# Optimization experiments

Measured on AMD Instinct MI355X. Metric: run time of the kernel, lower is better.

The kernel has to match this reference:

```python
import jax, jax.numpy as jnp
import numpy as np

NUM_CAPSULE = 32
DIM_CAPSULE = 16
ROUTINGS = 3
EPS = 1e-7        # K.epsilon()
L2_EPS = 1e-12    # tf.nn.l2_normalize epsilon


def squash(x, axis=-1):
    s = jnp.sum(jnp.square(x), axis=axis, keepdims=True) + EPS
    scale = jnp.sqrt(s) / (0.5 + s)
    return scale * x


def setup_inputs() -> dict:
    key = jax.random.key(0)
    k1, k2 = jax.random.split(key)
    B, N_in, D_in = 64, 2048, 64
    u_vecs = jax.random.normal(k1, (B, N_in, D_in), dtype=jnp.float32)
    # glorot-ish scale for the 1x1 conv kernel (1, D_in, num_capsule*dim_capsule)
    kernel = jax.random.normal(k2, (1, D_in, NUM_CAPSULE * DIM_CAPSULE), dtype=jnp.float32)
    kernel = kernel * np.sqrt(2.0 / (D_in + NUM_CAPSULE * DIM_CAPSULE)).astype(np.float32)
    return {"u_vecs": u_vecs, "kernel": kernel}


def reference(u_vecs, kernel):
    B, N_in, D_in = u_vecs.shape
    # K.conv1d with kernel_size=1 == matmul along the feature dim
    u_hat = jnp.einsum('bnd,dm->bnm', u_vecs, kernel[0])
    # (B, N_in, num_cap, dim_cap) -> (B, num_cap, N_in, dim_cap)
    u_hat = u_hat.reshape(B, N_in, NUM_CAPSULE, DIM_CAPSULE).transpose(0, 2, 1, 3)

    b = jnp.zeros((B, NUM_CAPSULE, N_in), dtype=u_hat.dtype)
    o = None
    for i in range(ROUTINGS):
        c = jax.nn.softmax(b, axis=1)                 # softmax over output capsules
        o = jnp.einsum('bin,binj->bij', c, u_hat)     # (B, num_cap, dim_cap)
        if i < ROUTINGS - 1:
            norm = jnp.sqrt(jnp.maximum(jnp.sum(jnp.square(o), axis=-1, keepdims=True), L2_EPS))
            o = o / norm                              # K.l2_normalize(o, -1)
            b = jnp.einsum('bij,binj->bin', o, u_hat)  # b = <v, u_hat> (non-accumulating)
    return squash(o)
```

## Files before the change

kernel.cpp:

```cpp
#include <hip/hip_runtime.h>
#include <hip/hip_bf16.h>


#define BB 64
#define NN 2048
#define DD 64
#define II 32

typedef __attribute__((ext_vector_type(8)))  short bf16x8;
typedef __attribute__((ext_vector_type(16))) float f32x16;

__device__ __forceinline__ short f2bf(float f) {
    __hip_bfloat16 h = __float2bfloat16(f);
    return *reinterpret_cast<short*>(&h);
}
__device__ __forceinline__ float bf2f(short s) {
    __hip_bfloat16 h = *reinterpret_cast<__hip_bfloat16*>(&s);
    return __bfloat162float(h);
}

__global__ __launch_bounds__(512) void kall(const float* __restrict__ u,
                                            const float* __restrict__ W,
                                            float* __restrict__ out) {
    int b = blockIdx.x;
    int tid = threadIdx.x;
    int wv = tid >> 6;
    int l = tid & 63, h = l >> 5, ln = l & 31;
    int ii = tid >> 4, jj0 = tid & 15;

    __shared__ unsigned short ush[8][2048];
    __shared__ unsigned short usl[8][2048];
    __shared__ float cslab[8][II * 33];
    __shared__ float tlds[II][65];
    __shared__ float wlds[II][68];
    __shared__ float slds[8][DD];
    __shared__ float ssum[DD];
    __shared__ float osh[II][16];

    const float* ubase = u + (size_t)b * NN * DD;

    {
        const float4* up = reinterpret_cast<const float4*>(ubase + (size_t)wv * 256 * DD);
        int r0 = l >> 4, c4 = l & 15;
        float4 a0 = {0.f, 0.f, 0.f, 0.f};
        #pragma unroll 8
        for (int s = 0; s < 64; ++s) {
            float4 v = up[(s * 4 + r0) * 16 + c4];
            a0.x += v.x; a0.y += v.y; a0.z += v.z; a0.w += v.w;
        }
        #pragma unroll
        for (int off = 16; off <= 32; off <<= 1) {
            a0.x += __shfl_xor(a0.x, off);
            a0.y += __shfl_xor(a0.y, off);
            a0.z += __shfl_xor(a0.z, off);
            a0.w += __shfl_xor(a0.w, off);
        }
        if (l < 16) *reinterpret_cast<float4*>(&slds[wv][l * 4]) = a0;
    }
    for (int k = tid; k < II * 65; k += 512) (&tlds[0][0])[k] = 0.f;
    __syncthreads();

    if (tid < DD) {
        float a = 0.f;
        #pragma unroll
        for (int wq = 0; wq < 8; ++wq) a += slds[wq][tid];
        ssum[tid] = a;
    }
    __syncthreads();
    {
        float o = 0.f;
        #pragma unroll 8
        for (int d = 0; d < DD; ++d) o += ssum[d] * W[d * 512 + ii * 16 + jj0];
        o *= (1.0f / 32.0f);
        float ss = o * o;
        #pragma unroll
        for (int off = 8; off >= 1; off >>= 1) ss += __shfl_xor(ss, off, 16);
        osh[ii][jj0] = o / sqrtf(fmaxf(ss, 1e-12f));
    }
    __syncthreads();
    #pragma unroll
    for (int k = 0; k < 4; ++k) {
        int d = jj0 + 16 * k;
        float acc = 0.f;
        #pragma unroll
        for (int j2 = 0; j2 < 16; ++j2)
            acc += W[d * 512 + ii * 16 + j2] * osh[ii][j2];
        wlds[ii][d] = acc;
    }
    __syncthreads();

    for (int it = 0; it < 2; ++it) {
        bf16x8 Aw[4];
        #pragma unroll
        for (int kt = 0; kt < 4; ++kt) {
            const float* p = &wlds[ln][kt * 16 + h * 8];
            #pragma unroll
            for (int e2 = 0; e2 < 8; ++e2) Aw[kt][e2] = f2bf(p[e2]);
        }
        f32x16 G0, G1;
        #pragma unroll
        for (int r = 0; r < 16; ++r) { G0[r] = 0.f; G1[r] = 0.f; }

        for (int tt = 0; tt < 8; ++tt) {
            int n0 = wv * 256 + tt * 32;
            bf16x8 Bh[4], Bl[4];
            #pragma unroll
            for (int kt = 0; kt < 4; ++kt) {
                const float4* p = reinterpret_cast<const float4*>(
                    ubase + (size_t)(n0 + ln) * DD + kt * 16 + h * 8);
                float4 v0 = p[0], v1 = p[1];
                float vf[8] = {v0.x, v0.y, v0.z, v0.w, v1.x, v1.y, v1.z, v1.w};
                #pragma unroll
                for (int e2 = 0; e2 < 8; ++e2) {
                    short hi = f2bf(vf[e2]);
                    Bh[kt][e2] = hi;
                    Bl[kt][e2] = f2bf(vf[e2] - bf2f(hi));
                }
                int d0 = kt * 16 + h * 8;
                int idx = ln * 64 + (d0 ^ ((ln & 7) << 3));
                *reinterpret_cast<bf16x8*>(&ush[wv][idx]) = Bh[kt];
                *reinterpret_cast<bf16x8*>(&usl[wv][idx]) = Bl[kt];
            }
            f32x16 S;
            #pragma unroll
            for (int r = 0; r < 16; ++r) S[r] = 0.f;
            #pragma unroll
            for (int kt = 0; kt < 4; ++kt)
                S = __builtin_amdgcn_mfma_f32_32x32x16_bf16(Aw[kt], Bh[kt], S, 0, 0, 0);
            float m = S[0];
            #pragma unroll
            for (int r = 1; r < 16; ++r) m = fmaxf(m, S[r]);
            m = fmaxf(m, __shfl_xor(m, 32));
            float sum = 0.f, e[16];
            #pragma unroll
            for (int r = 0; r < 16; ++r) { e[r] = __expf(S[r] - m); sum += e[r]; }
            sum += __shfl_xor(sum, 32);
            float inv = 1.f / sum;
            #pragma unroll
            for (int r = 0; r < 16; ++r) {
                int irow = (r & 3) + 8 * (r >> 2) + 4 * h;
                cslab[wv][ln * 33 + irow] = e[r] * inv;
            }
            #pragma unroll
            for (int t2 = 0; t2 < 2; ++t2) {
                bf16x8 Ah, Al;
                #pragma unroll
                for (int q = 0; q < 8; ++q) {
                    float cv = cslab[wv][(t2 * 16 + h * 8 + q) * 33 + ln];
                    short hi = f2bf(cv);
                    Ah[q] = hi;
                    Al[q] = f2bf(cv - bf2f(hi));
                }
                #pragma unroll
                for (int Nt = 0; Nt < 2; ++Nt) {
                    bf16x8 B2h, B2l;
                    #pragma unroll
                    for (int q = 0; q < 8; ++q) {
                        int row = t2 * 16 + h * 8 + q;
                        int idx = row * 64 + ((Nt * 32 + ln) ^ ((row & 7) << 3));
                        B2h[q] = (short)ush[wv][idx];
                        B2l[q] = (short)usl[wv][idx];
                    }
                    if (Nt == 0) {
                        G0 = __builtin_amdgcn_mfma_f32_32x32x16_bf16(Ah, B2h, G0, 0, 0, 0);
                        G0 = __builtin_amdgcn_mfma_f32_32x32x16_bf16(Al, B2h, G0, 0, 0, 0);
                        G0 = __builtin_amdgcn_mfma_f32_32x32x16_bf16(Ah, B2l, G0, 0, 0, 0);
                    } else {
                        G1 = __builtin_amdgcn_mfma_f32_32x32x16_bf16(Ah, B2h, G1, 0, 0, 0);
                        G1 = __builtin_amdgcn_mfma_f32_32x32x16_bf16(Al, B2h, G1, 0, 0, 0);
                        G1 = __builtin_amdgcn_mfma_f32_32x32x16_bf16(Ah, B2l, G1, 0, 0, 0);
                    }
                }
            }
        }
        #pragma unroll
        for (int r = 0; r < 16; ++r) {
            int irow = (r & 3) + 8 * (r >> 2) + 4 * h;
            atomicAdd(&tlds[irow][ln],      G0[r]);
            atomicAdd(&tlds[irow][32 + ln], G1[r]);
        }
        __syncthreads();

        float o = 0.f;
        #pragma unroll 8
        for (int d = 0; d < DD; ++d) o += tlds[ii][d] * W[d * 512 + ii * 16 + jj0];
        float ss = o * o;
        #pragma unroll
        for (int off = 8; off >= 1; off >>= 1) ss += __shfl_xor(ss, off, 16);

        if (it == 0) {
            float ov = o / sqrtf(fmaxf(ss, 1e-12f));
            __syncthreads();
            osh[ii][jj0] = ov;
            __syncthreads();
            #pragma unroll
            for (int k = 0; k < 4; ++k) {
                int d = jj0 + 16 * k;
                float acc = 0.f;
                #pragma unroll
                for (int j2 = 0; j2 < 16; ++j2)
                    acc += W[d * 512 + ii * 16 + j2] * osh[ii][j2];
                wlds[ii][d] = acc;
            }
            for (int k = tid; k < II * 65; k += 512) (&tlds[0][0])[k] = 0.f;
            __syncthreads();
        } else {
            float s2 = ss + 1e-7f;
            float scale = sqrtf(s2) / (0.5f + s2);
            out[(size_t)b * 512 + tid] = scale * o;
        }
    }
}

extern "C" void kernel_launch(void* const* d_in, const int* in_sizes, int n_in,
                              void* d_out, int out_size, void* d_ws, size_t ws_size,
                              hipStream_t stream) {
    const float* u = (const float*)d_in[0];
    const float* W = (const float*)d_in[1];
    float* out = (float*)d_out;
    (void)d_ws; (void)ws_size;

    kall<<<BB, 512, 0, stream>>>(u, W, out);
}
```

Baseline: 100.8 us.

## Split each batch across four cooperative blocks with grid sync reductions

Launches a cooperative kernel with 256 blocks (four per batch element), each handling 512 of the 2048 input rows. Partial column sums and per-iteration routing accumulators go through global workspace and are combined after grid.sync. This targets the low occupancy of the original 64-block launch on a GPU with many more CUs. The cost is three grid-wide barriers plus extra global traffic, and the old kernel is kept as a fallback if the cooperative launch fails. Global loads in the main loop are also batched before conversion.

```diff
diff --git a/kernel.cpp b/kernel.cpp
--- a/kernel.cpp
+++ b/kernel.cpp
@@ -1,5 +1,8 @@
 #include <hip/hip_runtime.h>
 #include <hip/hip_bf16.h>
+#include <hip/hip_cooperative_groups.h>
+
+namespace cg = cooperative_groups;
 
 
 #define BB 64
@@ -19,10 +22,15 @@
     return __bfloat162float(h);
 }
 
-__global__ __launch_bounds__(512) void kall(const float* __restrict__ u,
-                                            const float* __restrict__ W,
-                                            float* __restrict__ out) {
-    int b = blockIdx.x;
+__global__ __launch_bounds__(512) void kco(const float* __restrict__ u,
+                                           const float* __restrict__ W,
+                                           float* __restrict__ out,
+                                           float* __restrict__ sglob,
+                                           float* __restrict__ tglob) {
+    cg::grid_group grid = cg::this_grid();
+
+    int blk = blockIdx.x;
+    int b = blk >> 2, q = blk & 3;
     int tid = threadIdx.x;
     int wv = tid >> 6;
     int l = tid & 63, h = l >> 5, ln = l & 31;
@@ -38,13 +46,14 @@
     __shared__ float osh[II][16];
 
     const float* ubase = u + (size_t)b * NN * DD;
+    int rbase = q * 512 + wv * 64;
 
     {
-        const float4* up = reinterpret_cast<const float4*>(ubase + (size_t)wv * 256 * DD);
+        const float4* up = reinterpret_cast<const float4*>(ubase + (size_t)rbase * DD);
         int r0 = l >> 4, c4 = l & 15;
         float4 a0 = {0.f, 0.f, 0.f, 0.f};
-        #pragma unroll 8
-        for (int s = 0; s < 64; ++s) {
+        #pragma unroll
+        for (int s = 0; s < 16; ++s) {
             float4 v = up[(s * 4 + r0) * 16 + c4];
             a0.x += v.x; a0.y += v.y; a0.z += v.z; a0.w += v.w;
         }
@@ -57,13 +66,20 @@
         }
         if (l < 16) *reinterpret_cast<float4*>(&slds[wv][l * 4]) = a0;
     }
-    for (int k = tid; k < II * 65; k += 512) (&tlds[0][0])[k] = 0.f;
-    __syncthreads();
-
+    __syncthreads();
     if (tid < DD) {
         float a = 0.f;
         #pragma unroll
         for (int wq = 0; wq < 8; ++wq) a += slds[wq][tid];
+        sglob[(size_t)blk * DD + tid] = a;
+    }
+    __threadfence();
+    grid.sync();
+
+    if (tid < DD) {
+        float a = 0.f;
+        #pragma unroll
+        for (int q2 = 0; q2 < 4; ++q2) a += sglob[(size_t)(b * 4 + q2) * DD + tid];
         ssum[tid] = a;
     }
     __syncthreads();
@@ -101,15 +117,21 @@
         #pragma unroll
         for (int r = 0; r < 16; ++r) { G0[r] = 0.f; G1[r] = 0.f; }
 
-        for (int tt = 0; tt < 8; ++tt) {
-            int n0 = wv * 256 + tt * 32;
+        #pragma unroll
+        for (int tt = 0; tt < 2; ++tt) {
+            int n0 = rbase + tt * 32;
             bf16x8 Bh[4], Bl[4];
+            float4 v0[4], v1[4];
             #pragma unroll
             for (int kt = 0; kt < 4; ++kt) {
                 const float4* p = reinterpret_cast<const float4*>(
                     ubase + (size_t)(n0 + ln) * DD + kt * 16 + h * 8);
-                float4 v0 = p[0], v1 = p[1];
-                float vf[8] = {v0.x, v0.y, v0.z, v0.w, v1.x, v1.y, v1.z, v1.w};
+                v0[kt] = p[0]; v1[kt] = p[1];
+            }
+            #pragma unroll
+            for (int kt = 0; kt < 4; ++kt) {
+                float vf[8] = {v0[kt].x, v0[kt].y, v0[kt].z, v0[kt].w,
+                               v1[kt].x, v1[kt].y, v1[kt].z, v1[kt].w};
                 #pragma unroll
                 for (int e2 = 0; e2 < 8; ++e2) {
                     short hi = f2bf(vf[e2]);
@@ -145,21 +167,21 @@
             for (int t2 = 0; t2 < 2; ++t2) {
                 bf16x8 Ah, Al;
                 #pragma unroll
-                for (int q = 0; q < 8; ++q) {
-                    float cv = cslab[wv][(t2 * 16 + h * 8 + q) * 33 + ln];
+                for (int qq = 0; qq < 8; ++qq) {
+                    float cv = cslab[wv][(t2 * 16 + h * 8 + qq) * 33 + ln];
                     short hi = f2bf(cv);
-                    Ah[q] = hi;
-                    Al[q] = f2bf(cv - bf2f(hi));
+                    Ah[qq] = hi;
+                    Al[qq] = f2bf(cv - bf2f(hi));
                 }
                 #pragma unroll
                 for (int Nt = 0; Nt < 2; ++Nt) {
                     bf16x8 B2h, B2l;
                     #pragma unroll
-                    for (int q = 0; q < 8; ++q) {
-                        int row = t2 * 16 + h * 8 + q;
+                    for (int qq = 0; qq < 8; ++qq) {
+                        int row = t2 * 16 + h * 8 + qq;
                         int idx = row * 64 + ((Nt * 32 + ln) ^ ((row & 7) << 3));
-                        B2h[q] = (short)ush[wv][idx];
-                        B2l[q] = (short)usl[wv][idx];
+                        B2h[qq] = (short)ush[wv][idx];
+                        B2l[qq] = (short)usl[wv][idx];
                     }
                     if (Nt == 0) {
                         G0 = __builtin_amdgcn_mfma_f32_32x32x16_bf16(Ah, B2h, G0, 0, 0, 0);
@@ -173,6 +195,212 @@
                 }
             }
         }
+
+        for (int k = tid; k < II * 65; k += 512) (&tlds[0][0])[k] = 0.f;
+        __syncthreads();
+        #pragma unroll
+        for (int r = 0; r < 16; ++r) {
+            int irow = (r & 3) + 8 * (r >> 2) + 4 * h;
+            atomicAdd(&tlds[irow][ln],      G0[r]);
+            atomicAdd(&tlds[irow][32 + ln], G1[r]);
+        }
+        __syncthreads();
+        for (int k = tid; k < II * DD; k += 512)
+            tglob[(size_t)blk * (II * DD) + k] = tlds[k >> 6][k & 63];
+        __threadfence();
+        grid.sync();
+
+        for (int k = tid; k < II * DD; k += 512) {
+            float a = 0.f;
+            #pragma unroll
+            for (int q2 = 0; q2 < 4; ++q2)
+                a += tglob[(size_t)(b * 4 + q2) * (II * DD) + k];
+            tlds[k >> 6][k & 63] = a;
+        }
+        __syncthreads();
+        float o = 0.f;
+        #pragma unroll 8
+        for (int d = 0; d < DD; ++d) o += tlds[ii][d] * W[d * 512 + ii * 16 + jj0];
+        float ss = o * o;
+        #pragma unroll
+        for (int off = 8; off >= 1; off >>= 1) ss += __shfl_xor(ss, off, 16);
+
+        if (it == 0) {
+            float ov = o / sqrtf(fmaxf(ss, 1e-12f));
+            osh[ii][jj0] = ov;
+            __syncthreads();
+            #pragma unroll
+            for (int k = 0; k < 4; ++k) {
+                int d = jj0 + 16 * k;
+                float acc = 0.f;
+                #pragma unroll
+                for (int j2 = 0; j2 < 16; ++j2)
+                    acc += W[d * 512 + ii * 16 + j2] * osh[ii][j2];
+                wlds[ii][d] = acc;
+            }
+            __syncthreads();
+        } else if (q == 0) {
+            float s2 = ss + 1e-7f;
+            float scale = sqrtf(s2) / (0.5f + s2);
+            out[(size_t)b * 512 + tid] = scale * o;
+        }
+    }
+}
+
+__global__ __launch_bounds__(512) void kall(const float* __restrict__ u,
+                                            const float* __restrict__ W,
+                                            float* __restrict__ out) {
+    int b = blockIdx.x;
+    int tid = threadIdx.x;
+    int wv = tid >> 6;
+    int l = tid & 63, h = l >> 5, ln = l & 31;
+    int ii = tid >> 4, jj0 = tid & 15;
+
+    __shared__ unsigned short ush[8][2048];
+    __shared__ unsigned short usl[8][2048];
+    __shared__ float cslab[8][II * 33];
+    __shared__ float tlds[II][65];
+    __shared__ float wlds[II][68];
+    __shared__ float slds[8][DD];
+    __shared__ float ssum[DD];
+    __shared__ float osh[II][16];
+
+    const float* ubase = u + (size_t)b * NN * DD;
+
+    {
+        const float4* up = reinterpret_cast<const float4*>(ubase + (size_t)wv * 256 * DD);
+        int r0 = l >> 4, c4 = l & 15;
+        float4 a0 = {0.f, 0.f, 0.f, 0.f};
+        #pragma unroll 8
+        for (int s = 0; s < 64; ++s) {
+            float4 v = up[(s * 4 + r0) * 16 + c4];
+            a0.x += v.x; a0.y += v.y; a0.z += v.z; a0.w += v.w;
+        }
+        #pragma unroll
+        for (int off = 16; off <= 32; off <<= 1) {
+            a0.x += __shfl_xor(a0.x, off);
+            a0.y += __shfl_xor(a0.y, off);
+            a0.z += __shfl_xor(a0.z, off);
+            a0.w += __shfl_xor(a0.w, off);
+        }
+        if (l < 16) *reinterpret_cast<float4*>(&slds[wv][l * 4]) = a0;
+    }
+    for (int k = tid; k < II * 65; k += 512) (&tlds[0][0])[k] = 0.f;
+    __syncthreads();
+
+    if (tid < DD) {
+        float a = 0.f;
+        #pragma unroll
+        for (int wq = 0; wq < 8; ++wq) a += slds[wq][tid];
+        ssum[tid] = a;
+    }
+    __syncthreads();
+    {
+        float o = 0.f;
+        #pragma unroll 8
+        for (int d = 0; d < DD; ++d) o += ssum[d] * W[d * 512 + ii * 16 + jj0];
+        o *= (1.0f / 32.0f);
+        float ss = o * o;
+        #pragma unroll
+        for (int off = 8; off >= 1; off >>= 1) ss += __shfl_xor(ss, off, 16);
+        osh[ii][jj0] = o / sqrtf(fmaxf(ss, 1e-12f));
+    }
+    __syncthreads();
+    #pragma unroll
+    for (int k = 0; k < 4; ++k) {
+        int d = jj0 + 16 * k;
+        float acc = 0.f;
+        #pragma unroll
+        for (int j2 = 0; j2 < 16; ++j2)
+            acc += W[d * 512 + ii * 16 + j2] * osh[ii][j2];
+        wlds[ii][d] = acc;
+    }
+    __syncthreads();
+
+    for (int it = 0; it < 2; ++it) {
+        bf16x8 Aw[4];
+        #pragma unroll
+        for (int kt = 0; kt < 4; ++kt) {
+            const float* p = &wlds[ln][kt * 16 + h * 8];
+            #pragma unroll
+            for (int e2 = 0; e2 < 8; ++e2) Aw[kt][e2] = f2bf(p[e2]);
+        }
+        f32x16 G0, G1;
+        #pragma unroll
+        for (int r = 0; r < 16; ++r) { G0[r] = 0.f; G1[r] = 0.f; }
+
+        for (int tt = 0; tt < 8; ++tt) {
+            int n0 = wv * 256 + tt * 32;
+            bf16x8 Bh[4], Bl[4];
+            #pragma unroll
+            for (int kt = 0; kt < 4; ++kt) {
+                const float4* p = reinterpret_cast<const float4*>(
+                    ubase + (size_t)(n0 + ln) * DD + kt * 16 + h * 8);
+                float4 v0 = p[0], v1 = p[1];
+                float vf[8] = {v0.x, v0.y, v0.z, v0.w, v1.x, v1.y, v1.z, v1.w};
+                #pragma unroll
+                for (int e2 = 0; e2 < 8; ++e2) {
+                    short hi = f2bf(vf[e2]);
+                    Bh[kt][e2] = hi;
+                    Bl[kt][e2] = f2bf(vf[e2] - bf2f(hi));
+                }
+                int d0 = kt * 16 + h * 8;
+                int idx = ln * 64 + (d0 ^ ((ln & 7) << 3));
+                *reinterpret_cast<bf16x8*>(&ush[wv][idx]) = Bh[kt];
+                *reinterpret_cast<bf16x8*>(&usl[wv][idx]) = Bl[kt];
+            }
+            f32x16 S;
+            #pragma unroll
+            for (int r = 0; r < 16; ++r) S[r] = 0.f;
+            #pragma unroll
+            for (int kt = 0; kt < 4; ++kt)
+                S = __builtin_amdgcn_mfma_f32_32x32x16_bf16(Aw[kt], Bh[kt], S, 0, 0, 0);
+            float m = S[0];
+            #pragma unroll
+            for (int r = 1; r < 16; ++r) m = fmaxf(m, S[r]);
+            m = fmaxf(m, __shfl_xor(m, 32));
+            float sum = 0.f, e[16];
+            #pragma unroll
+            for (int r = 0; r < 16; ++r) { e[r] = __expf(S[r] - m); sum += e[r]; }
+            sum += __shfl_xor(sum, 32);
+            float inv = 1.f / sum;
+            #pragma unroll
+            for (int r = 0; r < 16; ++r) {
+                int irow = (r & 3) + 8 * (r >> 2) + 4 * h;
+                cslab[wv][ln * 33 + irow] = e[r] * inv;
+            }
+            #pragma unroll
+            for (int t2 = 0; t2 < 2; ++t2) {
+                bf16x8 Ah, Al;
+                #pragma unroll
+                for (int qq = 0; qq < 8; ++qq) {
+                    float cv = cslab[wv][(t2 * 16 + h * 8 + qq) * 33 + ln];
+                    short hi = f2bf(cv);
+                    Ah[qq] = hi;
+                    Al[qq] = f2bf(cv - bf2f(hi));
+                }
+                #pragma unroll
+                for (int Nt = 0; Nt < 2; ++Nt) {
+                    bf16x8 B2h, B2l;
+                    #pragma unroll
+                    for (int qq = 0; qq < 8; ++qq) {
+                        int row = t2 * 16 + h * 8 + qq;
+                        int idx = row * 64 + ((Nt * 32 + ln) ^ ((row & 7) << 3));
+                        B2h[qq] = (short)ush[wv][idx];
+                        B2l[qq] = (short)usl[wv][idx];
+                    }
+                    if (Nt == 0) {
+                        G0 = __builtin_amdgcn_mfma_f32_32x32x16_bf16(Ah, B2h, G0, 0, 0, 0);
+                        G0 = __builtin_amdgcn_mfma_f32_32x32x16_bf16(Al, B2h, G0, 0, 0, 0);
+                        G0 = __builtin_amdgcn_mfma_f32_32x32x16_bf16(Ah, B2l, G0, 0, 0, 0);
+                    } else {
+                        G1 = __builtin_amdgcn_mfma_f32_32x32x16_bf16(Ah, B2h, G1, 0, 0, 0);
+                        G1 = __builtin_amdgcn_mfma_f32_32x32x16_bf16(Al, B2h, G1, 0, 0, 0);
+                        G1 = __builtin_amdgcn_mfma_f32_32x32x16_bf16(Ah, B2l, G1, 0, 0, 0);
+                    }
+                }
+            }
+        }
         #pragma unroll
         for (int r = 0; r < 16; ++r) {
             int irow = (r & 3) + 8 * (r >> 2) + 4 * h;
@@ -218,7 +446,15 @@
     const float* u = (const float*)d_in[0];
     const float* W = (const float*)d_in[1];
     float* out = (float*)d_out;
-    (void)d_ws; (void)ws_size;
-
-    kall<<<BB, 512, 0, stream>>>(u, W, out);
+    float* ws = (float*)d_ws;
+
+    float* sglob = ws;
+    float* tglob = ws + 256 * DD;
+
+    void* args[] = {(void*)&u, (void*)&W, (void*)&out, (void*)&sglob, (void*)&tglob};
+    hipError_t e = hipLaunchCooperativeKernel((const void*)kco, dim3(256), dim3(512),
+                                              args, 0, stream);
+    if (e != hipSuccess) {
+        kall<<<BB, 512, 0, stream>>>(u, W, out);
+    }
 }
```

Result: slower. 278.1 us (+175.8%).

## Double block to 1024 threads and drop LDS staging of u tiles

Applied to the files above, without the earlier changes.

Raises threads per block from 512 to 1024, so each of 16 waves handles 128 input rows instead of 256. The bf16 hi/lo LDS copies of u and the softmax staging slab are removed. The A and B operands now swap roles in the logit MFMA, and the softmax runs across lanes with shuffles. The second GEMM reads u straight from global memory with strided scalar loads and splits it into hi/lo on the fly. This cuts LDS use and adds parallelism per batch, at the cost of more shuffles and less coalesced global reloads.

```diff
diff --git a/kernel.cpp b/kernel.cpp
--- a/kernel.cpp
+++ b/kernel.cpp
@@ -6,6 +6,8 @@
 #define NN 2048
 #define DD 64
 #define II 32
+#define WPB 16
+#define TPB 1024
 
 typedef __attribute__((ext_vector_type(8)))  short bf16x8;
 typedef __attribute__((ext_vector_type(16))) float f32x16;
@@ -19,33 +21,30 @@
     return __bfloat162float(h);
 }
 
-__global__ __launch_bounds__(512) void kall(const float* __restrict__ u,
+__global__ __launch_bounds__(TPB) void kone(const float* __restrict__ u,
                                             const float* __restrict__ W,
                                             float* __restrict__ out) {
     int b = blockIdx.x;
     int tid = threadIdx.x;
     int wv = tid >> 6;
     int l = tid & 63, h = l >> 5, ln = l & 31;
-    int ii = tid >> 4, jj0 = tid & 15;
-
-    __shared__ unsigned short ush[8][2048];
-    __shared__ unsigned short usl[8][2048];
-    __shared__ float cslab[8][II * 33];
+    int ii = (tid >> 4) & 31, jj0 = tid & 15;
+
     __shared__ float tlds[II][65];
     __shared__ float wlds[II][68];
-    __shared__ float slds[8][DD];
+    __shared__ float osh[II][16];
     __shared__ float ssum[DD];
-    __shared__ float osh[II][16];
 
     const float* ubase = u + (size_t)b * NN * DD;
 
     {
-        const float4* up = reinterpret_cast<const float4*>(ubase + (size_t)wv * 256 * DD);
+        const float4* up = reinterpret_cast<const float4*>(
+            ubase + (size_t)wv * 128 * DD);
         int r0 = l >> 4, c4 = l & 15;
         float4 a0 = {0.f, 0.f, 0.f, 0.f};
         #pragma unroll 8
-        for (int s = 0; s < 64; ++s) {
-            float4 v = up[(s * 4 + r0) * 16 + c4];
+        for (int s2 = 0; s2 < 32; ++s2) {
+            float4 v = up[(s2 * 4 + r0) * 16 + c4];
             a0.x += v.x; a0.y += v.y; a0.z += v.z; a0.w += v.w;
         }
         #pragma unroll
@@ -55,19 +54,20 @@
             a0.z += __shfl_xor(a0.z, off);
             a0.w += __shfl_xor(a0.w, off);
         }
-        if (l < 16) *reinterpret_cast<float4*>(&slds[wv][l * 4]) = a0;
-    }
-    for (int k = tid; k < II * 65; k += 512) (&tlds[0][0])[k] = 0.f;
-    __syncthreads();
-
+        if (l < 16)
+            reinterpret_cast<float4*>(&tlds[0][0])[wv * 16 + l] = a0;
+    }
+    __syncthreads();
     if (tid < DD) {
+        const float* slds = &tlds[0][0];
         float a = 0.f;
         #pragma unroll
-        for (int wq = 0; wq < 8; ++wq) a += slds[wq][tid];
+        for (int wq = 0; wq < WPB; ++wq) a += slds[wq * 64 + tid];
         ssum[tid] = a;
     }
     __syncthreads();
-    {
+
+    if (tid < 512) {
         float o = 0.f;
         #pragma unroll 8
         for (int d = 0; d < DD; ++d) o += ssum[d] * W[d * 512 + ii * 16 + jj0];
@@ -78,101 +78,101 @@
         osh[ii][jj0] = o / sqrtf(fmaxf(ss, 1e-12f));
     }
     __syncthreads();
-    #pragma unroll
-    for (int k = 0; k < 4; ++k) {
-        int d = jj0 + 16 * k;
-        float acc = 0.f;
-        #pragma unroll
-        for (int j2 = 0; j2 < 16; ++j2)
-            acc += W[d * 512 + ii * 16 + j2] * osh[ii][j2];
-        wlds[ii][d] = acc;
+    if (tid < 512) {
+        #pragma unroll
+        for (int k = 0; k < 4; ++k) {
+            int d = jj0 + 16 * k;
+            float acc = 0.f;
+            #pragma unroll
+            for (int j2 = 0; j2 < 16; ++j2)
+                acc += W[d * 512 + ii * 16 + j2] * osh[ii][j2];
+            wlds[ii][d] = acc;
+        }
+    } else {
+        for (int k = tid - 512; k < II * 65; k += 512) (&tlds[0][0])[k] = 0.f;
     }
     __syncthreads();
 
     for (int it = 0; it < 2; ++it) {
-        bf16x8 Aw[4];
-        #pragma unroll
-        for (int kt = 0; kt < 4; ++kt) {
-            const float* p = &wlds[ln][kt * 16 + h * 8];
-            #pragma unroll
-            for (int e2 = 0; e2 < 8; ++e2) Aw[kt][e2] = f2bf(p[e2]);
-        }
         f32x16 G0, G1;
         #pragma unroll
         for (int r = 0; r < 16; ++r) { G0[r] = 0.f; G1[r] = 0.f; }
 
-        for (int tt = 0; tt < 8; ++tt) {
-            int n0 = wv * 256 + tt * 32;
-            bf16x8 Bh[4], Bl[4];
+        #pragma unroll
+        for (int tt = 0; tt < 4; ++tt) {
+            int n0 = wv * 128 + tt * 32;
+
+            f32x16 S;
+            #pragma unroll
+            for (int r = 0; r < 16; ++r) S[r] = 0.f;
             #pragma unroll
             for (int kt = 0; kt < 4; ++kt) {
-                const float4* p = reinterpret_cast<const float4*>(
-                    ubase + (size_t)(n0 + ln) * DD + kt * 16 + h * 8);
-                float4 v0 = p[0], v1 = p[1];
-                float vf[8] = {v0.x, v0.y, v0.z, v0.w, v1.x, v1.y, v1.z, v1.w};
-                #pragma unroll
-                for (int e2 = 0; e2 < 8; ++e2) {
-                    short hi = f2bf(vf[e2]);
-                    Bh[kt][e2] = hi;
-                    Bl[kt][e2] = f2bf(vf[e2] - bf2f(hi));
+                int d0 = kt * 16 + h * 8;
+                const float4* pa = reinterpret_cast<const float4*>(
+                    ubase + (size_t)(n0 + ln) * DD + d0);
+                const float4* pb = reinterpret_cast<const float4*>(&wlds[ln][d0]);
+                float4 a0 = pa[0], a1 = pa[1];
+                float4 b0 = pb[0], b1 = pb[1];
+                bf16x8 A, Bv;
+                A[0]=f2bf(a0.x); A[1]=f2bf(a0.y); A[2]=f2bf(a0.z); A[3]=f2bf(a0.w);
+                A[4]=f2bf(a1.x); A[5]=f2bf(a1.y); A[6]=f2bf(a1.z); A[7]=f2bf(a1.w);
+                Bv[0]=f2bf(b0.x); Bv[1]=f2bf(b0.y); Bv[2]=f2bf(b0.z); Bv[3]=f2bf(b0.w);
+                Bv[4]=f2bf(b1.x); Bv[5]=f2bf(b1.y); Bv[6]=f2bf(b1.z); Bv[7]=f2bf(b1.w);
+                S = __builtin_amdgcn_mfma_f32_32x32x16_bf16(A, Bv, S, 0, 0, 0);
+            }
+
+            float c[16];
+            #pragma unroll
+            for (int r = 0; r < 16; ++r) {
+                float m = S[r];
+                #pragma unroll
+                for (int off = 1; off <= 16; off <<= 1)
+                    m = fmaxf(m, __shfl_xor(m, off));
+                float e = __expf(S[r] - m);
+                float s = e;
+                #pragma unroll
+                for (int off = 1; off <= 16; off <<= 1)
+                    s += __shfl_xor(s, off);
+                c[r] = e / s;
+            }
+
+            #pragma unroll
+            for (int t2 = 0; t2 < 2; ++t2) {
+                float pc[8];
+                #pragma unroll
+                for (int qq = 0; qq < 8; ++qq) pc[qq] = __shfl_xor(c[8 * t2 + qq], 32);
+                bf16x8 Ah, Al;
+                #pragma unroll
+                for (int j = 0; j < 8; ++j) {
+                    float av = ((j >> 2) == h) ? c[8 * t2 + j] : pc[j ^ 4];
+                    short hi = f2bf(av);
+                    Ah[j] = hi;
+                    Al[j] = f2bf(av - bf2f(hi));
                 }
-                int d0 = kt * 16 + h * 8;
-                int idx = ln * 64 + (d0 ^ ((ln & 7) << 3));
-                *reinterpret_cast<bf16x8*>(&ush[wv][idx]) = Bh[kt];
-                *reinterpret_cast<bf16x8*>(&usl[wv][idx]) = Bl[kt];
-            }
-            f32x16 S;
-            #pragma unroll
-            for (int r = 0; r < 16; ++r) S[r] = 0.f;
-            #pragma unroll
-            for (int kt = 0; kt < 4; ++kt)
-                S = __builtin_amdgcn_mfma_f32_32x32x16_bf16(Aw[kt], Bh[kt], S, 0, 0, 0);
-            float m = S[0];
-            #pragma unroll
-            for (int r = 1; r < 16; ++r) m = fmaxf(m, S[r]);
-            m = fmaxf(m, __shfl_xor(m, 32));
-            float sum = 0.f, e[16];
-            #pragma unroll
-            for (int r = 0; r < 16; ++r) { e[r] = __expf(S[r] - m); sum += e[r]; }
-            sum += __shfl_xor(sum, 32);
-            float inv = 1.f / sum;
-            #pragma unroll
-            for (int r = 0; r < 16; ++r) {
-                int irow = (r & 3) + 8 * (r >> 2) + 4 * h;
-                cslab[wv][ln * 33 + irow] = e[r] * inv;
-            }
-            #pragma unroll
-            for (int t2 = 0; t2 < 2; ++t2) {
-                bf16x8 Ah, Al;
-                #pragma unroll
-                for (int q = 0; q < 8; ++q) {
-                    float cv = cslab[wv][(t2 * 16 + h * 8 + q) * 33 + ln];
-                    short hi = f2bf(cv);
-                    Ah[q] = hi;
-                    Al[q] = f2bf(cv - bf2f(hi));
-                }
                 #pragma unroll
                 for (int Nt = 0; Nt < 2; ++Nt) {
-                    bf16x8 B2h, B2l;
+                    bf16x8 Bh, Bl;
                     #pragma unroll
-                    for (int q = 0; q < 8; ++q) {
-                        int row = t2 * 16 + h * 8 + q;
-                        int idx = row * 64 + ((Nt * 32 + ln) ^ ((row & 7) << 3));
-                        B2h[q] = (short)ush[wv][idx];
-                        B2l[q] = (short)usl[wv][idx];
+                    for (int j = 0; j < 8; ++j) {
+                        int n = t2 * 16 + h * 8 + j;
+                        float uv = ubase[(size_t)(n0 + n) * DD + Nt * 32 + ln];
+                        short hi = f2bf(uv);
+                        Bh[j] = hi;
+                        Bl[j] = f2bf(uv - bf2f(hi));
                     }
                     if (Nt == 0) {
-                        G0 = __builtin_amdgcn_mfma_f32_32x32x16_bf16(Ah, B2h, G0, 0, 0, 0);
-                        G0 = __builtin_amdgcn_mfma_f32_32x32x16_bf16(Al, B2h, G0, 0, 0, 0);
-                        G0 = __builtin_amdgcn_mfma_f32_32x32x16_bf16(Ah, B2l, G0, 0, 0, 0);
+                        G0 = __builtin_amdgcn_mfma_f32_32x32x16_bf16(Ah, Bh, G0, 0, 0, 0);
+                        G0 = __builtin_amdgcn_mfma_f32_32x32x16_bf16(Al, Bh, G0, 0, 0, 0);
+                        G0 = __builtin_amdgcn_mfma_f32_32x32x16_bf16(Ah, Bl, G0, 0, 0, 0);
                     } else {
-                        G1 = __builtin_amdgcn_mfma_f32_32x32x16_bf16(Ah, B2h, G1, 0, 0, 0);
-                        G1 = __builtin_amdgcn_mfma_f32_32x32x16_bf16(Al, B2h, G1, 0, 0, 0);
-                        G1 = __builtin_amdgcn_mfma_f32_32x32x16_bf16(Ah, B2l, G1, 0, 0, 0);
+                        G1 = __builtin_amdgcn_mfma_f32_32x32x16_bf16(Ah, Bh, G1, 0, 0, 0);
+                        G1 = __builtin_amdgcn_mfma_f32_32x32x16_bf16(Al, Bh, G1, 0, 0, 0);
+                        G1 = __builtin_amdgcn_mfma_f32_32x32x16_bf16(Ah, Bl, G1, 0, 0, 0);
                     }
                 }
             }
         }
+
         #pragma unroll
         for (int r = 0; r < 16; ++r) {
             int irow = (r & 3) + 8 * (r >> 2) + 4 * h;
@@ -181,30 +181,36 @@
         }
         __syncthreads();
 
-        float o = 0.f;
-        #pragma unroll 8
-        for (int d = 0; d < DD; ++d) o += tlds[ii][d] * W[d * 512 + ii * 16 + jj0];
-        float ss = o * o;
-        #pragma unroll
-        for (int off = 8; off >= 1; off >>= 1) ss += __shfl_xor(ss, off, 16);
+        float o = 0.f, ss = 0.f;
+        if (tid < 512) {
+            #pragma unroll 8
+            for (int d = 0; d < DD; ++d) o += tlds[ii][d] * W[d * 512 + ii * 16 + jj0];
+            ss = o * o;
+            #pragma unroll
+            for (int off = 8; off >= 1; off >>= 1) ss += __shfl_xor(ss, off, 16);
+        }
+        __syncthreads();
 
         if (it == 0) {
-            float ov = o / sqrtf(fmaxf(ss, 1e-12f));
+            if (tid < 512)
+                osh[ii][jj0] = o / sqrtf(fmaxf(ss, 1e-12f));
             __syncthreads();
-            osh[ii][jj0] = ov;
+            if (tid < 512) {
+                #pragma unroll
+                for (int k = 0; k < 4; ++k) {
+                    int d = jj0 + 16 * k;
+                    float acc = 0.f;
+                    #pragma unroll
+                    for (int j2 = 0; j2 < 16; ++j2)
+                        acc += W[d * 512 + ii * 16 + j2] * osh[ii][j2];
+                    wlds[ii][d] = acc;
+                }
+            } else {
+                for (int k = tid - 512; k < II * 65; k += 512)
+                    (&tlds[0][0])[k] = 0.f;
+            }
             __syncthreads();
-            #pragma unroll
-            for (int k = 0; k < 4; ++k) {
-                int d = jj0 + 16 * k;
-                float acc = 0.f;
-                #pragma unroll
-                for (int j2 = 0; j2 < 16; ++j2)
-                    acc += W[d * 512 + ii * 16 + j2] * osh[ii][j2];
-                wlds[ii][d] = acc;
-            }
-            for (int k = tid; k < II * 65; k += 512) (&tlds[0][0])[k] = 0.f;
-            __syncthreads();
-        } else {
+        } else if (tid < 512) {
             float s2 = ss + 1e-7f;
             float scale = sqrtf(s2) / (0.5f + s2);
             out[(size_t)b * 512 + tid] = scale * o;
@@ -220,5 +226,5 @@
     float* out = (float*)d_out;
     (void)d_ws; (void)ws_size;
 
-    kall<<<BB, 512, 0, stream>>>(u, W, out);
-}
+    kone<<<BB, TPB, 0, stream>>>(u, W, out);
+}
```

New measurement: 240.4 us. 2.38x slower.

## Split column-sum into wide pre-kernel and prefetch u tiles in routing loop

Applied to the files above, without the earlier changes.

The first-iteration column sum of u over N is moved out of the 64-block fused kernel into a separate 2048-block kernel that writes per-chunk partial sums to workspace; the main kernel then reduces 32 partials per batch. The main routing loop is fully unrolled and software-pipelined, loading the next 32-row u tile into registers while the current one is converted and multiplied. The aim is to use the whole GPU for the first full read of u instead of only 64 CUs, and to hide global load latency in the routing passes. In exchange it adds a second launch, a workspace round trip, and higher register pressure from the prefetch buffers.

```diff
diff --git a/kernel.cpp b/kernel.cpp
--- a/kernel.cpp
+++ b/kernel.cpp
@@ -19,9 +19,36 @@
     return __bfloat162float(h);
 }
 
-__global__ __launch_bounds__(512) void kall(const float* __restrict__ u,
-                                            const float* __restrict__ W,
-                                            float* __restrict__ out) {
+__global__ __launch_bounds__(256) void ksum(const float* __restrict__ u,
+                                            float* __restrict__ spart) {
+    int b = blockIdx.y, cb = blockIdx.x;
+    int tid = threadIdx.x, cg = tid & 15, rr = tid >> 4;
+    const float4* up = reinterpret_cast<const float4*>(
+        u + ((size_t)b * NN + (size_t)cb * 64 + rr) * DD) + cg;
+    float4 a = {0.f, 0.f, 0.f, 0.f};
+    #pragma unroll
+    for (int k = 0; k < 4; ++k) {
+        float4 v = up[(size_t)k * 16 * (DD / 4)];
+        a.x += v.x; a.y += v.y; a.z += v.z; a.w += v.w;
+    }
+    __shared__ float4 red[16][16];
+    red[rr][cg] = a;
+    __syncthreads();
+    if (rr == 0) {
+        float4 s = red[0][cg];
+        #pragma unroll
+        for (int r = 1; r < 16; ++r) {
+            s.x += red[r][cg].x; s.y += red[r][cg].y;
+            s.z += red[r][cg].z; s.w += red[r][cg].w;
+        }
+        reinterpret_cast<float4*>(spart + ((size_t)cb * BB + b) * DD)[cg] = s;
+    }
+}
+
+__global__ __launch_bounds__(512) void kf(const float* __restrict__ u,
+                                          const float* __restrict__ W,
+                                          const float* __restrict__ spart,
+                                          float* __restrict__ out) {
     int b = blockIdx.x;
     int tid = threadIdx.x;
     int wv = tid >> 6;
@@ -33,39 +60,19 @@
     __shared__ float cslab[8][II * 33];
     __shared__ float tlds[II][65];
     __shared__ float wlds[II][68];
-    __shared__ float slds[8][DD];
     __shared__ float ssum[DD];
     __shared__ float osh[II][16];
 
     const float* ubase = u + (size_t)b * NN * DD;
 
-    {
-        const float4* up = reinterpret_cast<const float4*>(ubase + (size_t)wv * 256 * DD);
-        int r0 = l >> 4, c4 = l & 15;
-        float4 a0 = {0.f, 0.f, 0.f, 0.f};
-        #pragma unroll 8
-        for (int s = 0; s < 64; ++s) {
-            float4 v = up[(s * 4 + r0) * 16 + c4];
-            a0.x += v.x; a0.y += v.y; a0.z += v.z; a0.w += v.w;
-        }
-        #pragma unroll
-        for (int off = 16; off <= 32; off <<= 1) {
-            a0.x += __shfl_xor(a0.x, off);
-            a0.y += __shfl_xor(a0.y, off);
-            a0.z += __shfl_xor(a0.z, off);
-            a0.w += __shfl_xor(a0.w, off);
-        }
-        if (l < 16) *reinterpret_cast<float4*>(&slds[wv][l * 4]) = a0;
-    }
-    for (int k = tid; k < II * 65; k += 512) (&tlds[0][0])[k] = 0.f;
-    __syncthreads();
-
     if (tid < DD) {
         float a = 0.f;
         #pragma unroll
-        for (int wq = 0; wq < 8; ++wq) a += slds[wq][tid];
+        for (int cb = 0; cb < 32; ++cb)
+            a += spart[((size_t)cb * BB + b) * DD + tid];
         ssum[tid] = a;
     }
+    for (int k = tid; k < II * 65; k += 512) (&tlds[0][0])[k] = 0.f;
     __syncthreads();
     {
         float o = 0.f;
@@ -101,14 +108,31 @@
         #pragma unroll
         for (int r = 0; r < 16; ++r) { G0[r] = 0.f; G1[r] = 0.f; }
 
+        float4 cur[8], nxt[8];
+        {
+            const float4* p = reinterpret_cast<const float4*>(
+                ubase + (size_t)(wv * 256 + ln) * DD);
+            #pragma unroll
+            for (int kt = 0; kt < 4; ++kt) {
+                cur[kt * 2 + 0] = p[kt * 4 + h * 2 + 0];
+                cur[kt * 2 + 1] = p[kt * 4 + h * 2 + 1];
+            }
+        }
+        #pragma unroll
         for (int tt = 0; tt < 8; ++tt) {
-            int n0 = wv * 256 + tt * 32;
+            if (tt < 7) {
+                const float4* p = reinterpret_cast<const float4*>(
+                    ubase + (size_t)(wv * 256 + (tt + 1) * 32 + ln) * DD);
+                #pragma unroll
+                for (int kt = 0; kt < 4; ++kt) {
+                    nxt[kt * 2 + 0] = p[kt * 4 + h * 2 + 0];
+                    nxt[kt * 2 + 1] = p[kt * 4 + h * 2 + 1];
+                }
+            }
             bf16x8 Bh[4], Bl[4];
             #pragma unroll
             for (int kt = 0; kt < 4; ++kt) {
-                const float4* p = reinterpret_cast<const float4*>(
-                    ubase + (size_t)(n0 + ln) * DD + kt * 16 + h * 8);
-                float4 v0 = p[0], v1 = p[1];
+                float4 v0 = cur[kt * 2 + 0], v1 = cur[kt * 2 + 1];
                 float vf[8] = {v0.x, v0.y, v0.z, v0.w, v1.x, v1.y, v1.z, v1.w};
                 #pragma unroll
                 for (int e2 = 0; e2 < 8; ++e2) {
@@ -145,21 +169,21 @@
             for (int t2 = 0; t2 < 2; ++t2) {
                 bf16x8 Ah, Al;
                 #pragma unroll
-                for (int q = 0; q < 8; ++q) {
-                    float cv = cslab[wv][(t2 * 16 + h * 8 + q) * 33 + ln];
+                for (int qq = 0; qq < 8; ++qq) {
+                    float cv = cslab[wv][(t2 * 16 + h * 8 + qq) * 33 + ln];
                     short hi = f2bf(cv);
-                    Ah[q] = hi;
-                    Al[q] = f2bf(cv - bf2f(hi));
+                    Ah[qq] = hi;
+                    Al[qq] = f2bf(cv - bf2f(hi));
                 }
                 #pragma unroll
                 for (int Nt = 0; Nt < 2; ++Nt) {
                     bf16x8 B2h, B2l;
                     #pragma unroll
-                    for (int q = 0; q < 8; ++q) {
-                        int row = t2 * 16 + h * 8 + q;
+                    for (int qq = 0; qq < 8; ++qq) {
+                        int row = t2 * 16 + h * 8 + qq;
                         int idx = row * 64 + ((Nt * 32 + ln) ^ ((row & 7) << 3));
-                        B2h[q] = (short)ush[wv][idx];
-                        B2l[q] = (short)usl[wv][idx];
+                        B2h[qq] = (short)ush[wv][idx];
+                        B2l[qq] = (short)usl[wv][idx];
                     }
                     if (Nt == 0) {
                         G0 = __builtin_amdgcn_mfma_f32_32x32x16_bf16(Ah, B2h, G0, 0, 0, 0);
@@ -172,7 +196,10 @@
                     }
                 }
             }
-        }
+            #pragma unroll
+            for (int q = 0; q < 8; ++q) cur[q] = nxt[q];
+        }
+
         #pragma unroll
         for (int r = 0; r < 16; ++r) {
             int irow = (r & 3) + 8 * (r >> 2) + 4 * h;
@@ -218,7 +245,10 @@
     const float* u = (const float*)d_in[0];
     const float* W = (const float*)d_in[1];
     float* out = (float*)d_out;
-    (void)d_ws; (void)ws_size;
-
-    kall<<<BB, 512, 0, stream>>>(u, W, out);
-}
+    float* ws = (float*)d_ws;
+
+    float* spart = ws;
+
+    ksum<<<dim3(32, BB), 256, 0, stream>>>(u, spart);
+    kf<<<BB, 512, 0, stream>>>(u, W, spart, out);
+}
```

Result: slower. 140.3 us (+39.1%).
